# Kernel tuning notes

Measured on AMD Instinct MI355X. Metric: run time of the kernel, lower is better.

The kernel has to match this reference:

```python
import jax, jax.numpy as jnp
import numpy as np

K = 5            # SplineConv kernel_size per dim, dim=3
KC = K ** 3      # 125 weight matrices
N0, N1, N2, N3 = 32768, 8192, 2048, 512   # node counts per pooling level (8 graphs)
E0, E1, E2, E3 = 262144, 65536, 16384, 4096
B = 8
NV = B * 8       # dense 2x2x2 voxel grid per graph -> fc1 input 8*256


def spline_conv(x, edge_index, pseudo, W, root, bias):
    # degree-1 (linear) open B-spline convolution, mean aggregation,
    # plus root weight and bias (torch SplineConv defaults).
    src, dst = edge_index[0], edge_index[1]
    N, Cin = x.shape
    Kc, _, Cout = W.shape
    E = src.shape[0]
    v = pseudo * (K - 1)                               # [E,3]
    lo = jnp.clip(jnp.floor(v), 0, K - 2)
    frac = v - lo                                      # [E,3]
    lo = lo.astype(jnp.int32)
    bits = jnp.array([[(s >> d) & 1 for d in range(3)] for s in range(8)], dtype=jnp.int32)  # [8,3]
    idx = lo[:, None, :] + bits[None]                  # [E,8,3] corner grid indices
    w = jnp.where(bits[None] == 1, frac[:, None, :], 1.0 - frac[:, None, :])
    bw = jnp.prod(w, axis=-1)                          # [E,8] basis weights (sum to 1)
    kidx = idx[..., 0] + K * idx[..., 1] + K * K * idx[..., 2]  # [E,8] flat kernel index
    if N * Kc < E * Cin:
        # project every node through all 125 kernels, then gather per edge-corner
        P = jnp.einsum('nc,kco->nko', x, W)            # [N,125,Cout]
        msg = jnp.sum(bw[..., None] * P[src[:, None], kidx], axis=1)  # [E,Cout]
    else:
        # gather weight matrices per edge-corner (cheaper when Cin small)
        xs = x[src]                                    # [E,Cin]
        msg = jnp.zeros((E, Cout), x.dtype)
        for s in range(8):                             # fixed 8 corners of trilinear basis
            msg = msg + bw[:, s, None] * jnp.einsum('ec,eco->eo', xs, W[kidx[:, s]])
    agg = jax.ops.segment_sum(msg, dst, num_segments=N)
    deg = jax.ops.segment_sum(jnp.ones((E,), x.dtype), dst, num_segments=N)
    return agg / jnp.maximum(deg, 1.0)[:, None] + x @ root + bias


def pool_max(x, cluster, n_out):
    out = jax.ops.segment_max(x, cluster, num_segments=n_out)
    return jnp.where(jnp.isfinite(out), out, 0.0)      # empty voxels -> 0


def setup_inputs():
    key = jax.random.key(0)
    ks = iter(jax.random.split(key, 40))
    inp = {"x": jax.random.normal(next(ks), (N0, 1), jnp.float32)}
    levels = [(E0, N0, N1), (E1, N1, N2), (E2, N2, N3), (E3, N3, NV)]
    for l, (E, N, Nn) in enumerate(levels, start=1):
        inp[f"edge_index{l}"] = jax.random.randint(next(ks), (2, E), 0, N)
        inp[f"pseudo{l}"] = jax.random.uniform(next(ks), (E, 3), dtype=jnp.float32)
        inp[f"cluster{l}"] = jax.random.randint(next(ks), (N,), 0, Nn)
    chans = [(1, 32), (32, 64), (64, 128), (128, 256)]
    for l, (ci, co) in enumerate(chans, start=1):
        inp[f"W{l}"] = jax.random.normal(next(ks), (KC, ci, co), jnp.float32) / np.sqrt(ci * 8.0)
        inp[f"root{l}"] = jax.random.normal(next(ks), (ci, co), jnp.float32) / np.sqrt(float(ci))
        inp[f"b{l}"] = jnp.zeros((co,), jnp.float32)
    inp["fc1_w"] = jax.random.normal(next(ks), (2048, 512), jnp.float32) / np.sqrt(2048.0)
    inp["fc1_b"] = jnp.zeros((512,), jnp.float32)
    inp["fc2_w"] = jax.random.normal(next(ks), (512, 10), jnp.float32) / np.sqrt(512.0)
    inp["fc2_b"] = jnp.zeros((10,), jnp.float32)
    return inp


def reference(x, edge_index1, pseudo1, cluster1, edge_index2, pseudo2, cluster2,
              edge_index3, pseudo3, cluster3, edge_index4, pseudo4, cluster4,
              W1, root1, b1, W2, root2, b2, W3, root3, b3, W4, root4, b4,
              fc1_w, fc1_b, fc2_w, fc2_b):
    h = jax.nn.elu(spline_conv(x, edge_index1, pseudo1, W1, root1, b1))
    h = pool_max(h, cluster1, N1)                      # sparse voxel max pool 0.02
    h = jax.nn.elu(spline_conv(h, edge_index2, pseudo2, W2, root2, b2))
    h = pool_max(h, cluster2, N2)                      # sparse voxel max pool 0.04
    h = jax.nn.elu(spline_conv(h, edge_index3, pseudo3, W3, root3, b3))
    h = pool_max(h, cluster3, N3)                      # sparse voxel max pool 0.08
    h = jax.nn.elu(spline_conv(h, edge_index4, pseudo4, W4, root4, b4))
    h = pool_max(h, cluster4, NV)                      # dense 2x2x2 voxel max pool
    h = h.reshape(B, 8 * 256)
    h = jax.nn.elu(h @ fc1_w + fc1_b)                  # dropout is identity in eval mode
    return jax.nn.log_softmax(h @ fc2_w + fc2_b, axis=1)
```

## Files before the change

kernel.cpp:

```cpp
#include <hip/hip_runtime.h>

typedef __attribute__((ext_vector_type(8))) short bf16x8;
typedef __attribute__((ext_vector_type(4))) float f32x4;
typedef __attribute__((ext_vector_type(8))) unsigned short us8;

#define DEVI __device__ __forceinline__

#define MAXW2 1088
#define MAXW3 640
#define MAXW4 512


DEVI unsigned enc_pool(float f) {
  unsigned u = __float_as_uint(f);
  return (u & 0x80000000u) ? ~u : (u | 0x80000000u);
}
DEVI float dec_pool(unsigned k) {
  if (k == 0u) return 0.0f;
  return __uint_as_float((k & 0x80000000u) ? (k ^ 0x80000000u) : ~k);
}
DEVI float eluf(float x) { return x > 0.0f ? x : expm1f(x); }
DEVI unsigned short to_bf16(float f) {
  unsigned u = __float_as_uint(f);
  return (unsigned short)((u + 0x7FFFu + ((u >> 16) & 1u)) >> 16);
}

DEVI int cell_of(const float* __restrict__ ps, int e) {
  int cell = 0;
#pragma unroll
  for (int d = 0; d < 3; ++d) {
    float v = ps[e * 3 + d] * 4.0f;
    float fl = fminf(fmaxf(floorf(v), 0.0f), 3.0f);
    cell |= ((int)fl) << (2 * d);
  }
  return cell;
}

template <int CIN, int COUT>
DEVI void convw(const float* __restrict__ W, unsigned short* __restrict__ P, int idx) {
  constexpr int MAT = CIN * COUT;
  int k = idx / MAT, off = idx % MAT;
  int j = off & 7, g = (off >> 3) & 3;
  int rem = off >> 5;
  int n = rem % COUT, kb = rem / COUT;
  int c = kb * 32 + g * 8 + j;
  P[idx] = to_bf16(W[(k * CIN + c) * COUT + n]);
}

__global__ __launch_bounds__(256) void sc_prep(
    const float* __restrict__ W2, const float* __restrict__ W3, const float* __restrict__ W4,
    unsigned short* __restrict__ P2, unsigned short* __restrict__ P3, unsigned short* __restrict__ P4,
    const int* __restrict__ ei2, const float* __restrict__ ps2,
    const int* __restrict__ ei3, const float* __restrict__ ps3,
    const int* __restrict__ ei4, const float* __restrict__ ps4,
    unsigned* __restrict__ bc2, unsigned* __restrict__ bc3, unsigned* __restrict__ bc4,
    unsigned* __restrict__ deg2, unsigned* __restrict__ deg3, unsigned* __restrict__ deg4,
    const float* __restrict__ x, const int* __restrict__ ei1, const float* __restrict__ ps1,
    const float* __restrict__ W1, float* __restrict__ agg1, unsigned* __restrict__ deg1) {
  __shared__ unsigned hist[64];
  int b = blockIdx.x, t = threadIdx.x;
  if (b < 1000) { convw<32, 64>(W2, P2, b * 256 + t); return; }
  b -= 1000;
  if (b < 4000) { convw<64, 128>(W3, P3, b * 256 + t); return; }
  b -= 4000;
  if (b < 16000) { convw<128, 256>(W4, P4, b * 256 + t); return; }
  b -= 16000;
  if (b < 336) {
    const int* ei; const float* ps; unsigned *bc, *deg; int E, blk, NB;
    if (b < 256)      { ei = ei2; ps = ps2; bc = bc2; deg = deg2; E = 65536; blk = b;       NB = 256; }
    else if (b < 320) { ei = ei3; ps = ps3; bc = bc3; deg = deg3; E = 16384; blk = b - 256; NB = 64;  }
    else              { ei = ei4; ps = ps4; bc = bc4; deg = deg4; E = 4096;  blk = b - 320; NB = 16;  }
    if (t < 64) hist[t] = 0;
    __syncthreads();
    int e = blk * 256 + t;
    atomicAdd(&hist[cell_of(ps, e)], 1u);
    atomicAdd(deg + ei[E + e], 1u);
    __syncthreads();
    if (t < 64) bc[(size_t)t * NB + blk] = hist[t];
    return;
  }
  b -= 336;
  int tid = b * 256 + t;
  int e = tid >> 5, o = tid & 31;
  int ebit = t & 32;
  int src = ei1[e], dst = ei1[262144 + e];
  float f[3]; int lo[3];
#pragma unroll
  for (int d = 0; d < 3; ++d) {
    float v = ps1[e * 3 + d] * 4.0f;
    float fl = fminf(fmaxf(floorf(v), 0.0f), 3.0f);
    lo[d] = (int)fl;
    f[d] = v - fl;
  }
  int so = o & 7;
  int c0 = so & 1, c1 = (so >> 1) & 1, c2 = (so >> 2) & 1;
  float bw_own = (c0 ? f[0] : 1.0f - f[0]) * (c1 ? f[1] : 1.0f - f[1]) *
                 (c2 ? f[2] : 1.0f - f[2]);
  int k_own = (lo[0] + c0) + 5 * (lo[1] + c1) + 25 * (lo[2] + c2);
  float acc = 0.f;
#pragma unroll
  for (int s = 0; s < 8; ++s) {
    float bws = __shfl(bw_own, ebit + s);
    int ks = __shfl(k_own, ebit + s);
    acc += bws * W1[ks * 32 + o];
  }
  atomicAdd(agg1 + dst * 32 + o, x[src] * acc);
  if (o == 0) atomicAdd(deg1 + dst, 1u);
}

__global__ __launch_bounds__(1024) void sc_scan_all(
    const unsigned* __restrict__ bc2, const unsigned* __restrict__ bc3,
    const unsigned* __restrict__ bc4,
    unsigned* __restrict__ bb2, unsigned* __restrict__ bb3, unsigned* __restrict__ bb4,
    unsigned* __restrict__ cnt2, unsigned* __restrict__ cnt3, unsigned* __restrict__ cnt4,
    unsigned* __restrict__ base2, unsigned* __restrict__ base3, unsigned* __restrict__ base4,
    unsigned* __restrict__ wt2, unsigned* __restrict__ wt3, unsigned* __restrict__ wt4) {
  __shared__ unsigned tot[3][64];
  __shared__ unsigned sbs[3][64];
  int t = threadIdx.x, w = t >> 6, lane = t & 63;
#pragma unroll
  for (int lvl = 0; lvl < 3; ++lvl) {
    const unsigned* bc = lvl == 0 ? bc2 : lvl == 1 ? bc3 : bc4;
    unsigned* bb = lvl == 0 ? bb2 : lvl == 1 ? bb3 : bb4;
    int NB = lvl == 0 ? 256 : lvl == 1 ? 64 : 16;
    for (int c = w; c < 64; c += 16) {
      unsigned cellsum = 0;
      for (int sub = 0; sub * 64 < NB; ++sub) {
        int bi = sub * 64 + lane;
        unsigned v = (bi < NB) ? bc[c * NB + bi] : 0u;
        int incl = (int)v;
#pragma unroll
        for (int d = 1; d < 64; d <<= 1) {
          int tv = __shfl_up(incl, d);
          if (lane >= d) incl += tv;
        }
        if (bi < NB) bb[c * NB + bi] = cellsum + (unsigned)incl - v;
        cellsum += (unsigned)__shfl(incl, 63);
      }
      if (lane == 0) tot[lvl][c] = cellsum;
    }
  }
  __syncthreads();
  if (w < 3) {
    unsigned* cnt = w == 0 ? cnt2 : w == 1 ? cnt3 : cnt4;
    unsigned* bs  = w == 0 ? base2 : w == 1 ? base3 : base4;
    unsigned* wt  = w == 0 ? wt2 : w == 1 ? wt3 : wt4;
    int NSP  = w == 0 ? 1 : w == 1 ? 2 : 4;
    int MAXW = w == 0 ? MAXW2 : w == 1 ? MAXW3 : MAXW4;
    unsigned v = tot[w][lane];
    int incl = (int)v;
#pragma unroll
    for (int d = 1; d < 64; d <<= 1) {
      int tv = __shfl_up(incl, d);
      if (lane >= d) incl += tv;
    }
    unsigned excl = (unsigned)incl - v;
    sbs[w][lane] = excl;
    cnt[lane] = v;
    bs[lane] = excl;
    int nch = (int)((v + 63) >> 6);
    int cscan = nch;
#pragma unroll
    for (int d = 1; d < 64; d <<= 1) {
      int tv = __shfl_up(cscan, d);
      if (lane >= d) cscan += tv;
    }
    int cbase = cscan - nch;
    int CT = __shfl(cscan, 63);
    for (int ch = 0; ch < nch; ++ch)
      for (int ns = 0; ns < NSP; ++ns)
        wt[(cbase + ch) * NSP + ns] = ((unsigned)lane << 16) | ((unsigned)ch << 8) | (unsigned)ns;
    for (int i = CT * NSP + lane; i < MAXW; i += 64) wt[i] = 0xFFFFFFFFu;
  }
  __syncthreads();
  for (int i = t; i < 64 * 256; i += 1024) bb2[i] += sbs[0][i >> 8];
  for (int i = t; i < 64 * 64; i += 1024)  bb3[i] += sbs[1][i >> 6];
  for (int i = t; i < 64 * 16; i += 1024)  bb4[i] += sbs[2][i >> 4];
}

__global__ __launch_bounds__(256) void sc_rank_fin1(
    const int* __restrict__ ei2, const float* __restrict__ ps2,
    const int* __restrict__ ei3, const float* __restrict__ ps3,
    const int* __restrict__ ei4, const float* __restrict__ ps4,
    const unsigned* __restrict__ bb2, const unsigned* __restrict__ bb3,
    const unsigned* __restrict__ bb4,
    int* __restrict__ eid2, int* __restrict__ eid3, int* __restrict__ eid4,
    int* __restrict__ dst2, int* __restrict__ dst3, int* __restrict__ dst4,
    const float* __restrict__ x, const float* __restrict__ agg1,
    const unsigned* __restrict__ deg1, const float* __restrict__ root1,
    const float* __restrict__ b1, const int* __restrict__ cl1,
    unsigned* __restrict__ pe1) {
  __shared__ unsigned hist[64];
  int b = blockIdx.x, t = threadIdx.x;
  if (b < 336) {
    const int* ei; const float* ps; const unsigned* bb; int *eid, *dsts; int E, blk, NB;
    if (b < 256)      { ei = ei2; ps = ps2; bb = bb2; eid = eid2; dsts = dst2; E = 65536; blk = b;       NB = 256; }
    else if (b < 320) { ei = ei3; ps = ps3; bb = bb3; eid = eid3; dsts = dst3; E = 16384; blk = b - 256; NB = 64;  }
    else              { ei = ei4; ps = ps4; bb = bb4; eid = eid4; dsts = dst4; E = 4096;  blk = b - 320; NB = 16;  }
    if (t < 64) hist[t] = 0;
    __syncthreads();
    int e = blk * 256 + t;
    int cell = cell_of(ps, e);
    unsigned r = atomicAdd(&hist[cell], 1u);
    int p = (int)(bb[cell * NB + blk] + r);
    eid[p] = e;
    dsts[p] = ei[E + e];
    return;
  }
  b -= 336;
  int tid = b * 256 + t;
  int n = tid >> 5, o = tid & 31;
  unsigned dv = deg1[n];
  float acc = agg1[tid] / (float)(dv ? dv : 1u) + b1[o] + x[n] * root1[o];
  atomicMax(pe1 + (size_t)cl1[n] * 32 + o, enc_pool(eluf(acc)));
}

template <int CIN, int COUT>
__global__ void sc_finpool(const unsigned* __restrict__ xenc, const float* __restrict__ agg,
                           const unsigned* __restrict__ deg, const float* __restrict__ root,
                           const float* __restrict__ bias, const int* __restrict__ cluster,
                           unsigned* __restrict__ pe_out, int N) {
  int tid = blockIdx.x * blockDim.x + threadIdx.x;
  if (tid >= N * COUT) return;
  int n = tid / COUT, o = tid % COUT;
  unsigned dv = deg[n];
  float acc = agg[tid] / (float)(dv ? dv : 1u) + bias[o];
#pragma unroll 4
  for (int c = 0; c < CIN; ++c)
    acc += dec_pool(xenc[n * CIN + c]) * root[c * COUT + o];
  atomicMax(pe_out + (size_t)cluster[n] * COUT + o, enc_pool(eluf(acc)));
}

template <int CIN, int COUT, int NSP>
DEVI void gemm_impl(const int* __restrict__ ei, const float* __restrict__ ps,
                    const unsigned* __restrict__ xenc, const int* __restrict__ eid,
                    const unsigned short* __restrict__ Wp,
                    const unsigned* __restrict__ cnt, const unsigned* __restrict__ base,
                    const unsigned* __restrict__ wtab, const int* __restrict__ dsts,
                    float* __restrict__ agg) {
  constexpr int K = 8 * CIN;
  constexpr int NCOL = COUT / NSP;
  constexpr int NT = NCOL / 16;
  constexpr int UPT = NCOL / 32;
  constexpr int NPASS = K / 64;
  __shared__ __attribute__((aligned(16))) unsigned char lds[2 * NCOL * 80];
  __shared__ __attribute__((aligned(16))) unsigned short ldsA[64][72];
  __shared__ float s_bw[64][8];
  __shared__ int s_src[64];
  unsigned u = wtab[blockIdx.x];
  if (u == 0xFFFFFFFFu) return;
  int cell = u >> 16, chunk = (u >> 8) & 255, nsl = u & 255;
  int n0 = nsl * NCOL;
  int m = (int)cnt[cell], cb = (int)base[cell];
  int row0 = chunk * 64;
  int tid = threadIdx.x;
  int wv = tid >> 6, lane = tid & 63, g4 = lane >> 4, ln = lane & 15;
  int lo0 = cell & 3, lo1 = (cell >> 2) & 3, lo2 = cell >> 4;
  if (tid < 64) {
    int ridx = cb + min(row0 + tid, m - 1);
    int e = eid[ridx];
    s_src[tid] = ei[e];
    float f[3];
#pragma unroll
    for (int d = 0; d < 3; ++d) {
      float v = ps[e * 3 + d] * 4.0f;
      float fl = fminf(fmaxf(floorf(v), 0.0f), 3.0f);
      f[d] = v - fl;
    }
#pragma unroll
    for (int s = 0; s < 8; ++s) {
      int b0 = s & 1, b1 = (s >> 1) & 1, b2 = (s >> 2) & 1;
      s_bw[tid][s] = (b0 ? f[0] : 1.0f - f[0]) * (b1 ? f[1] : 1.0f - f[1]) *
                     (b2 ? f[2] : 1.0f - f[2]);
    }
  }
  f32x4 acc[NT];
#pragma unroll
  for (int t = 0; t < NT; ++t) acc[t] = (f32x4){0.f, 0.f, 0.f, 0.f};
  for (int pass = 0; pass < NPASS; ++pass) {
    int k0 = pass * 64;
    __syncthreads();
#pragma unroll
    for (int i = 0; i < UPT; ++i) {
      int u16 = tid + i * 256;
      int grp = u16 / (4 * NCOL), win = u16 % (4 * NCOL);
      int kg = k0 + grp * 32;
      int s = kg / CIN, kb = (kg % CIN) >> 5;
      int b0 = s & 1, b1 = (s >> 1) & 1, b2 = (s >> 2) & 1;
      int mat = (lo0 + b0) + 5 * (lo1 + b1) + 25 * (lo2 + b2);
      const us8* srcp = (const us8*)(Wp + (size_t)mat * (CIN * COUT) +
                                     (size_t)(kb * COUT * 4 + n0 * 4 + win) * 8);
      int r = grp * NCOL + (win >> 2), gg = win & 3;
      *(us8*)(lds + r * 80 + gg * 16) = *srcp;
    }
    {
      int r = tid >> 2, q = tid & 3;
      int kg = k0 + q * 16;
      int sidx = kg / CIN;
      int c0 = kg & (CIN - 1);
      float bwv = s_bw[r][sidx];
      const uint4* xp = (const uint4*)(xenc + (size_t)s_src[r] * CIN + c0);
      uint4 xa = xp[0], xb = xp[1];
      us8 o0;
      o0[0] = to_bf16(bwv * dec_pool(xa.x)); o0[1] = to_bf16(bwv * dec_pool(xa.y));
      o0[2] = to_bf16(bwv * dec_pool(xa.z)); o0[3] = to_bf16(bwv * dec_pool(xa.w));
      o0[4] = to_bf16(bwv * dec_pool(xb.x)); o0[5] = to_bf16(bwv * dec_pool(xb.y));
      o0[6] = to_bf16(bwv * dec_pool(xb.z)); o0[7] = to_bf16(bwv * dec_pool(xb.w));
      uint4 xc = xp[2], xd = xp[3];
      us8 o1;
      o1[0] = to_bf16(bwv * dec_pool(xc.x)); o1[1] = to_bf16(bwv * dec_pool(xc.y));
      o1[2] = to_bf16(bwv * dec_pool(xc.z)); o1[3] = to_bf16(bwv * dec_pool(xc.w));
      o1[4] = to_bf16(bwv * dec_pool(xd.x)); o1[5] = to_bf16(bwv * dec_pool(xd.y));
      o1[6] = to_bf16(bwv * dec_pool(xd.z)); o1[7] = to_bf16(bwv * dec_pool(xd.w));
      *(us8*)&ldsA[r][q * 16] = o0;
      *(us8*)&ldsA[r][q * 16 + 8] = o1;
    }
    __syncthreads();
#pragma unroll
    for (int kk = 0; kk < 2; ++kk) {
      bf16x8 af = *(const bf16x8*)&ldsA[wv * 16 + ln][kk * 32 + g4 * 8];
#pragma unroll
      for (int t = 0; t < NT; ++t) {
        int r = kk * NCOL + t * 16 + ln;
        bf16x8 bfr = *(const bf16x8*)(lds + r * 80 + g4 * 16);
        acc[t] = __builtin_amdgcn_mfma_f32_16x16x32_bf16(af, bfr, acc[t], 0, 0, 0);
      }
    }
  }
  int row_b = row0 + wv * 16 + g4 * 4;
  int dstv[4];
#pragma unroll
  for (int r4 = 0; r4 < 4; ++r4)
    dstv[r4] = (row_b + r4 < m) ? dsts[cb + row_b + r4] : -1;
#pragma unroll
  for (int t = 0; t < NT; ++t) {
#pragma unroll
    for (int r4 = 0; r4 < 4; ++r4) {
      if (dstv[r4] >= 0)
        atomicAdd(agg + (size_t)dstv[r4] * COUT + n0 + t * 16 + ln, acc[t][r4]);
    }
  }
}

__global__ __launch_bounds__(256) void sc_gemm_l2(
    const int* ei, const float* ps, const unsigned* xenc, const int* eid,
    const unsigned short* Wp, const unsigned* cnt, const unsigned* base,
    const unsigned* wtab, const int* dsts, float* agg) {
  gemm_impl<32, 64, 1>(ei, ps, xenc, eid, Wp, cnt, base, wtab, dsts, agg);
}
__global__ __launch_bounds__(256) void sc_gemm_l3(
    const int* ei, const float* ps, const unsigned* xenc, const int* eid,
    const unsigned short* Wp, const unsigned* cnt, const unsigned* base,
    const unsigned* wtab, const int* dsts, float* agg) {
  gemm_impl<64, 128, 2>(ei, ps, xenc, eid, Wp, cnt, base, wtab, dsts, agg);
}
__global__ __launch_bounds__(256) void sc_gemm_l4(
    const int* ei, const float* ps, const unsigned* xenc, const int* eid,
    const unsigned short* Wp, const unsigned* cnt, const unsigned* base,
    const unsigned* wtab, const int* dsts, float* agg) {
  gemm_impl<128, 256, 4>(ei, ps, xenc, eid, Wp, cnt, base, wtab, dsts, agg);
}

__global__ void sc_fc1(const unsigned* __restrict__ xenc, const float* __restrict__ w,
                       float* __restrict__ out) {
  __shared__ float sx[8][32];
  int t = threadIdx.x;
  int j = blockIdx.x * 256 + t;
  int c0 = blockIdx.y * 32;
  {
    int b = t >> 5, c = t & 31;
    sx[b][c] = dec_pool(xenc[b * 2048 + c0 + c]);
  }
  __syncthreads();
  float acc[8];
#pragma unroll
  for (int b = 0; b < 8; ++b) acc[b] = 0.f;
#pragma unroll 4
  for (int cc = 0; cc < 32; ++cc) {
    float wv = w[(size_t)(c0 + cc) * 512 + j];
#pragma unroll
    for (int b = 0; b < 8; ++b) acc[b] += sx[b][cc] * wv;
  }
#pragma unroll
  for (int b = 0; b < 8; ++b) atomicAdd(out + b * 512 + j, acc[b]);
}

__global__ void sc_fc2(const float* __restrict__ h, const float* __restrict__ b1,
                       const float* __restrict__ w2, const float* __restrict__ b2,
                       float* __restrict__ out) {
  int b = blockIdx.x;
  int lane = threadIdx.x;
  float part[10];
#pragma unroll
  for (int o = 0; o < 10; ++o) part[o] = 0.f;
  for (int k = 0; k < 8; ++k) {
    int c = k * 64 + lane;
    float v = eluf(h[b * 512 + c] + b1[c]);
#pragma unroll
    for (int o = 0; o < 10; ++o) part[o] += v * w2[c * 10 + o];
  }
#pragma unroll
  for (int o = 0; o < 10; ++o) {
#pragma unroll
    for (int d = 32; d > 0; d >>= 1) part[o] += __shfl_down(part[o], d);
  }
  if (lane == 0) {
    float z[10], mx = -1e30f;
#pragma unroll
    for (int o = 0; o < 10; ++o) { z[o] = part[o] + b2[o]; mx = fmaxf(mx, z[o]); }
    float sum = 0.f;
#pragma unroll
    for (int o = 0; o < 10; ++o) sum += expf(z[o] - mx);
    float lse = mx + logf(sum);
#pragma unroll
    for (int o = 0; o < 10; ++o) out[b * 10 + o] = z[o] - lse;
  }
}

extern "C" void kernel_launch(void* const* d_in, const int* in_sizes, int n_in,
                              void* d_out, int out_size, void* d_ws, size_t ws_size,
                              hipStream_t stream) {
  (void)in_sizes; (void)n_in; (void)out_size; (void)ws_size;
  const float* x    = (const float*)d_in[0];
  const int*   ei1  = (const int*)d_in[1];
  const float* ps1  = (const float*)d_in[2];
  const int*   cl1  = (const int*)d_in[3];
  const int*   ei2  = (const int*)d_in[4];
  const float* ps2  = (const float*)d_in[5];
  const int*   cl2  = (const int*)d_in[6];
  const int*   ei3  = (const int*)d_in[7];
  const float* ps3  = (const float*)d_in[8];
  const int*   cl3  = (const int*)d_in[9];
  const int*   ei4  = (const int*)d_in[10];
  const float* ps4  = (const float*)d_in[11];
  const int*   cl4  = (const int*)d_in[12];
  const float* W1   = (const float*)d_in[13];
  const float* root1= (const float*)d_in[14];
  const float* b1   = (const float*)d_in[15];
  const float* W2   = (const float*)d_in[16];
  const float* root2= (const float*)d_in[17];
  const float* b2   = (const float*)d_in[18];
  const float* W3   = (const float*)d_in[19];
  const float* root3= (const float*)d_in[20];
  const float* b3   = (const float*)d_in[21];
  const float* W4   = (const float*)d_in[22];
  const float* root4= (const float*)d_in[23];
  const float* b4   = (const float*)d_in[24];
  const float* fc1w = (const float*)d_in[25];
  const float* fc1b = (const float*)d_in[26];
  const float* fc2w = (const float*)d_in[27];
  const float* fc2b = (const float*)d_in[28];
  float* out = (float*)d_out;

  char* ws = (char*)d_ws;
  size_t off = 0;
  auto alloc = [&](size_t bytes) -> void* {
    void* p = ws + off;
    off = (off + bytes + 255) & ~(size_t)255;
    return p;
  };
  float*    agg1 = (float*)alloc(32768ull * 32 * 4);
  float*    agg2 = (float*)alloc(8192ull * 64 * 4);
  float*    agg3 = (float*)alloc(2048ull * 128 * 4);
  float*    agg4 = (float*)alloc(512ull * 256 * 4);
  unsigned* deg1 = (unsigned*)alloc(32768ull * 4);
  unsigned* deg2 = (unsigned*)alloc(8192ull * 4);
  unsigned* deg3 = (unsigned*)alloc(2048ull * 4);
  unsigned* deg4 = (unsigned*)alloc(512ull * 4);
  unsigned* pe1  = (unsigned*)alloc(8192ull * 32 * 4);
  unsigned* pe2  = (unsigned*)alloc(2048ull * 64 * 4);
  unsigned* pe3  = (unsigned*)alloc(512ull * 128 * 4);
  unsigned* pe4  = (unsigned*)alloc(64ull * 256 * 4);
  float*    fc1o = (float*)alloc(8ull * 512 * 4);
  size_t zero_bytes = off;
  unsigned* bc2   = (unsigned*)alloc(64ull * 256 * 4);
  unsigned* bc3   = (unsigned*)alloc(64ull * 64 * 4);
  unsigned* bc4   = (unsigned*)alloc(64ull * 16 * 4);
  unsigned* bb2   = (unsigned*)alloc(64ull * 256 * 4);
  unsigned* bb3   = (unsigned*)alloc(64ull * 64 * 4);
  unsigned* bb4   = (unsigned*)alloc(64ull * 16 * 4);
  unsigned* cnt2  = (unsigned*)alloc(64 * 4);
  unsigned* cnt3  = (unsigned*)alloc(64 * 4);
  unsigned* cnt4  = (unsigned*)alloc(64 * 4);
  unsigned* base2 = (unsigned*)alloc(64 * 4);
  unsigned* base3 = (unsigned*)alloc(64 * 4);
  unsigned* base4 = (unsigned*)alloc(64 * 4);
  unsigned* wt2   = (unsigned*)alloc(MAXW2 * 4);
  unsigned* wt3   = (unsigned*)alloc(MAXW3 * 4);
  unsigned* wt4   = (unsigned*)alloc(MAXW4 * 4);
  int* eid2 = (int*)alloc(65536ull * 4);
  int* eid3 = (int*)alloc(16384ull * 4);
  int* eid4 = (int*)alloc(4096ull * 4);
  int* dst2 = (int*)alloc(65536ull * 4);
  int* dst3 = (int*)alloc(16384ull * 4);
  int* dst4 = (int*)alloc(4096ull * 4);
  unsigned short* Wp2 = (unsigned short*)alloc(125ull * 32 * 64 * 2);
  unsigned short* Wp3 = (unsigned short*)alloc(125ull * 64 * 128 * 2);
  unsigned short* Wp4 = (unsigned short*)alloc(125ull * 128 * 256 * 2);

  hipMemsetAsync(d_ws, 0, zero_bytes, stream);
  sc_prep<<<54104, 256, 0, stream>>>(W2, W3, W4, Wp2, Wp3, Wp4,
                                     ei2, ps2, ei3, ps3, ei4, ps4,
                                     bc2, bc3, bc4, deg2, deg3, deg4,
                                     x, ei1, ps1, W1, agg1, deg1);
  sc_scan_all<<<1, 1024, 0, stream>>>(bc2, bc3, bc4, bb2, bb3, bb4,
                                      cnt2, cnt3, cnt4, base2, base3, base4,
                                      wt2, wt3, wt4);
  sc_rank_fin1<<<4432, 256, 0, stream>>>(ei2, ps2, ei3, ps3, ei4, ps4,
                                         bb2, bb3, bb4, eid2, eid3, eid4,
                                         dst2, dst3, dst4,
                                         x, agg1, deg1, root1, b1, cl1, pe1);

  sc_gemm_l2<<<MAXW2, 256, 0, stream>>>(ei2, ps2, pe1, eid2, Wp2, cnt2, base2, wt2, dst2, agg2);
  sc_finpool<32, 64><<<2048, 256, 0, stream>>>(pe1, agg2, deg2, root2, b2, cl2, pe2, 8192);

  sc_gemm_l3<<<MAXW3, 256, 0, stream>>>(ei3, ps3, pe2, eid3, Wp3, cnt3, base3, wt3, dst3, agg3);
  sc_finpool<64, 128><<<1024, 256, 0, stream>>>(pe2, agg3, deg3, root3, b3, cl3, pe3, 2048);

  sc_gemm_l4<<<MAXW4, 256, 0, stream>>>(ei4, ps4, pe3, eid4, Wp4, cnt4, base4, wt4, dst4, agg4);
  sc_finpool<128, 256><<<512, 256, 0, stream>>>(pe3, agg4, deg4, root4, b4, cl4, pe4, 512);

  sc_fc1<<<dim3(2, 64), 256, 0, stream>>>(pe4, fc1w, fc1o);
  sc_fc2<<<8, 64, 0, stream>>>(fc1o, fc1b, fc2w, fc2b, out);
}
```

Measured before the change: 195.4 us.

## Scatter layer-1 basis coefficients per node, then contract with W1 in finalize

```diff
diff --git a/kernel.cpp b/kernel.cpp
--- a/kernel.cpp
+++ b/kernel.cpp
@@ -36,35 +36,37 @@
   return cell;
 }
 
-template <int CIN, int COUT>
-DEVI void convw(const float* __restrict__ W, unsigned short* __restrict__ P, int idx) {
-  constexpr int MAT = CIN * COUT;
-  int k = idx / MAT, off = idx % MAT;
-  int j = off & 7, g = (off >> 3) & 3;
-  int rem = off >> 5;
+__global__ __launch_bounds__(256) void sc_convw(
+    const float* __restrict__ W2, const float* __restrict__ W3, const float* __restrict__ W4,
+    unsigned short* __restrict__ P2, unsigned short* __restrict__ P3, unsigned short* __restrict__ P4) {
+  int u = blockIdx.x * 256 + threadIdx.x;
+  const int U2 = 32000, U3 = 128000;
+  const float* W; unsigned short* P; int CIN, COUT;
+  if (u < U2)           { W = W2; P = P2; CIN = 32;  COUT = 64;  }
+  else if (u < U2 + U3) { u -= U2; W = W3; P = P3; CIN = 64;  COUT = 128; }
+  else                  { u -= U2 + U3; W = W4; P = P4; CIN = 128; COUT = 256; }
+  int MAT8 = CIN * COUT / 8;
+  int k = u / MAT8, off8 = u % MAT8;
+  int g = off8 & 3;
+  int rem = off8 >> 2;
   int n = rem % COUT, kb = rem / COUT;
-  int c = kb * 32 + g * 8 + j;
-  P[idx] = to_bf16(W[(k * CIN + c) * COUT + n]);
+  const float* ws = W + ((size_t)k * CIN + kb * 32 + g * 8) * COUT + n;
+  us8 o;
+#pragma unroll
+  for (int j = 0; j < 8; ++j) o[j] = to_bf16(ws[(size_t)j * COUT]);
+  *(us8*)(P + (size_t)u * 8) = o;
 }
 
 __global__ __launch_bounds__(256) void sc_prep(
-    const float* __restrict__ W2, const float* __restrict__ W3, const float* __restrict__ W4,
-    unsigned short* __restrict__ P2, unsigned short* __restrict__ P3, unsigned short* __restrict__ P4,
     const int* __restrict__ ei2, const float* __restrict__ ps2,
     const int* __restrict__ ei3, const float* __restrict__ ps3,
     const int* __restrict__ ei4, const float* __restrict__ ps4,
     unsigned* __restrict__ bc2, unsigned* __restrict__ bc3, unsigned* __restrict__ bc4,
     unsigned* __restrict__ deg2, unsigned* __restrict__ deg3, unsigned* __restrict__ deg4,
     const float* __restrict__ x, const int* __restrict__ ei1, const float* __restrict__ ps1,
-    const float* __restrict__ W1, float* __restrict__ agg1, unsigned* __restrict__ deg1) {
+    float* __restrict__ C, unsigned* __restrict__ deg1) {
   __shared__ unsigned hist[64];
   int b = blockIdx.x, t = threadIdx.x;
-  if (b < 1000) { convw<32, 64>(W2, P2, b * 256 + t); return; }
-  b -= 1000;
-  if (b < 4000) { convw<64, 128>(W3, P3, b * 256 + t); return; }
-  b -= 4000;
-  if (b < 16000) { convw<128, 256>(W4, P4, b * 256 + t); return; }
-  b -= 16000;
   if (b < 336) {
     const int* ei; const float* ps; unsigned *bc, *deg; int E, blk, NB;
     if (b < 256)      { ei = ei2; ps = ps2; bc = bc2; deg = deg2; E = 65536; blk = b;       NB = 256; }
@@ -81,8 +83,7 @@
   }
   b -= 336;
   int tid = b * 256 + t;
-  int e = tid >> 5, o = tid & 31;
-  int ebit = t & 32;
+  int e = tid >> 3, s = tid & 7;
   int src = ei1[e], dst = ei1[262144 + e];
   float f[3]; int lo[3];
 #pragma unroll
@@ -92,20 +93,12 @@
     lo[d] = (int)fl;
     f[d] = v - fl;
   }
-  int so = o & 7;
-  int c0 = so & 1, c1 = (so >> 1) & 1, c2 = (so >> 2) & 1;
-  float bw_own = (c0 ? f[0] : 1.0f - f[0]) * (c1 ? f[1] : 1.0f - f[1]) *
-                 (c2 ? f[2] : 1.0f - f[2]);
-  int k_own = (lo[0] + c0) + 5 * (lo[1] + c1) + 25 * (lo[2] + c2);
-  float acc = 0.f;
-#pragma unroll
-  for (int s = 0; s < 8; ++s) {
-    float bws = __shfl(bw_own, ebit + s);
-    int ks = __shfl(k_own, ebit + s);
-    acc += bws * W1[ks * 32 + o];
-  }
-  atomicAdd(agg1 + dst * 32 + o, x[src] * acc);
-  if (o == 0) atomicAdd(deg1 + dst, 1u);
+  int c0 = s & 1, c1 = (s >> 1) & 1, c2 = s >> 2;
+  float bw = (c0 ? f[0] : 1.0f - f[0]) * (c1 ? f[1] : 1.0f - f[1]) *
+             (c2 ? f[2] : 1.0f - f[2]);
+  int k = (lo[0] + c0) + 5 * (lo[1] + c1) + 25 * (lo[2] + c2);
+  atomicAdd(C + (size_t)dst * 128 + k, bw * x[src]);
+  if (s == 0) atomicAdd(deg1 + dst, 1u);
 }
 
 __global__ __launch_bounds__(1024) void sc_scan_all(
@@ -186,11 +179,13 @@
     const unsigned* __restrict__ bb4,
     int* __restrict__ eid2, int* __restrict__ eid3, int* __restrict__ eid4,
     int* __restrict__ dst2, int* __restrict__ dst3, int* __restrict__ dst4,
-    const float* __restrict__ x, const float* __restrict__ agg1,
+    const float* __restrict__ x, const float* __restrict__ C,
+    const float* __restrict__ W1,
     const unsigned* __restrict__ deg1, const float* __restrict__ root1,
     const float* __restrict__ b1, const int* __restrict__ cl1,
     unsigned* __restrict__ pe1) {
   __shared__ unsigned hist[64];
+  __shared__ float sW1[4000];
   int b = blockIdx.x, t = threadIdx.x;
   if (b < 336) {
     const int* ei; const float* ps; const unsigned* bb; int *eid, *dsts; int E, blk, NB;
@@ -208,10 +203,16 @@
     return;
   }
   b -= 336;
+  for (int i = t; i < 4000; i += 256) sW1[i] = W1[i];
+  __syncthreads();
   int tid = b * 256 + t;
   int n = tid >> 5, o = tid & 31;
+  const float* Cn = C + (size_t)n * 128;
+  float acc = 0.f;
+#pragma unroll 5
+  for (int k = 0; k < 125; ++k) acc += Cn[k] * sW1[k * 32 + o];
   unsigned dv = deg1[n];
-  float acc = agg1[tid] / (float)(dv ? dv : 1u) + b1[o] + x[n] * root1[o];
+  acc = acc / (float)(dv ? dv : 1u) + b1[o] + x[n] * root1[o];
   atomicMax(pe1 + (size_t)cl1[n] * 32 + o, enc_pool(eluf(acc)));
 }
 
@@ -459,7 +460,7 @@
     off = (off + bytes + 255) & ~(size_t)255;
     return p;
   };
-  float*    agg1 = (float*)alloc(32768ull * 32 * 4);
+  float*    C    = (float*)alloc(32768ull * 128 * 4);
   float*    agg2 = (float*)alloc(8192ull * 64 * 4);
   float*    agg3 = (float*)alloc(2048ull * 128 * 4);
   float*    agg4 = (float*)alloc(512ull * 256 * 4);
@@ -499,17 +500,17 @@
   unsigned short* Wp4 = (unsigned short*)alloc(125ull * 128 * 256 * 2);
 
   hipMemsetAsync(d_ws, 0, zero_bytes, stream);
-  sc_prep<<<54104, 256, 0, stream>>>(W2, W3, W4, Wp2, Wp3, Wp4,
-                                     ei2, ps2, ei3, ps3, ei4, ps4,
-                                     bc2, bc3, bc4, deg2, deg3, deg4,
-                                     x, ei1, ps1, W1, agg1, deg1);
+  sc_convw<<<2625, 256, 0, stream>>>(W2, W3, W4, Wp2, Wp3, Wp4);
+  sc_prep<<<8528, 256, 0, stream>>>(ei2, ps2, ei3, ps3, ei4, ps4,
+                                    bc2, bc3, bc4, deg2, deg3, deg4,
+                                    x, ei1, ps1, C, deg1);
   sc_scan_all<<<1, 1024, 0, stream>>>(bc2, bc3, bc4, bb2, bb3, bb4,
                                       cnt2, cnt3, cnt4, base2, base3, base4,
                                       wt2, wt3, wt4);
   sc_rank_fin1<<<4432, 256, 0, stream>>>(ei2, ps2, ei3, ps3, ei4, ps4,
                                          bb2, bb3, bb4, eid2, eid3, eid4,
                                          dst2, dst3, dst4,
-                                         x, agg1, deg1, root1, b1, cl1, pe1);
+                                         x, C, W1, deg1, root1, b1, cl1, pe1);
 
   sc_gemm_l2<<<MAXW2, 256, 0, stream>>>(ei2, ps2, pe1, eid2, Wp2, cnt2, base2, wt2, dst2, agg2);
   sc_finpool<32, 64><<<2048, 256, 0, stream>>>(pe1, agg2, deg2, root2, b2, cl2, pe2, 8192);
```

Measured after the change: 217.4 us. 1.11x slower.
